# Kernel tuning notes

Measured on AMD Instinct MI355X. Metric: run time of the kernel, lower is better.

Reference implementation:

```python
import jax, jax.numpy as jnp
import numpy as np

EPS = 1e-8

def _conv(x, w, b=None):
    # NCHW conv, stride 1, SAME padding (k=3, pad=1)
    y = jax.lax.conv_general_dilated(x, w, (1, 1), 'SAME',
                                     dimension_numbers=('NCHW', 'OIHW', 'NCHW'))
    if b is not None:
        y = y + b[None, :, None, None]
    return y

def setup_inputs() -> dict:
    key = jax.random.key(0)
    ks = jax.random.split(key, 6)
    B, C, H, W = 512, 1024, 8, 8
    return {
        'x': jax.random.normal(ks[0], (B, C, H, W), jnp.float32),
        'w1_1': jax.random.normal(ks[1], (1, 1, 3, 3), jnp.float32) * 0.1,
        'w5': jax.random.normal(ks[2], (4, 2, 3, 3), jnp.float32) * 0.1,
        'b5': jax.random.normal(ks[3], (4,), jnp.float32) * 0.1,
        'w6': jax.random.normal(ks[4], (1, 4, 3, 3), jnp.float32) * 0.1,
        'b6': jax.random.normal(ks[5], (1,), jnp.float32) * 0.1,
    }

def reference(x, w1_1, w5, b5, w6, b6):
    B, C, H, W = x.shape  # H == W == 8 by module construction
    m = jnp.max(x, axis=1, keepdims=True)  # [B,1,H,W] channel max
    # 2x2 non-overlapping windows, torch unfold layout -> [B,1,(H/2)*(W/2),4]
    win = m.reshape(B, 1, H // 2, 2, W // 2, 2)
    win = win.transpose(0, 1, 2, 4, 3, 5).reshape(B, 1, (H // 2) * (W // 2), 4)
    # probabilistic pooling: clean inf/nan/negatives, sample per window
    winc = jnp.where(jnp.isinf(win) | jnp.isnan(win) | (win < 0), EPS, win)
    skey = jax.random.key(1)
    idx = jax.random.categorical(skey, winc, axis=-1)  # softmax(winc) multinomial
    mo2 = jnp.take_along_axis(winc, idx[..., None], axis=-1)[..., 0]
    mo2 = mo2.reshape(B, 1, H // 2, W // 2)
    # adaptive max/avg pool (4,4) on 8x8 == 2x2 pooling, reuse windows
    mo3 = win.max(axis=-1).reshape(B, 1, H // 2, W // 2)
    ao4 = win.mean(axis=-1).reshape(B, 1, H // 2, W // 2)
    out2 = 0.1 * mo2 + 0.6 * mo3 + 0.3 * ao4
    out2 = _conv(out2, w1_1)  # bias-free 1->1 conv
    out2 = jax.image.resize(out2, (B, 1, H, W), method='bilinear')  # align_corners=False
    out1 = jnp.concatenate([m, out2], axis=1)  # [B,2,H,W]
    gate = jax.nn.sigmoid(_conv(jax.nn.relu(_conv(out1, w5, b5)), w6, b6))  # [B,1,H,W]
    return jax.nn.relu(x * gate)
```

## Files before the change

kernel.cpp:

```cpp
#include <hip/hip_runtime.h>
#include <math.h>

#define C_DIM 1024
#define HW 64
#define NT_A 512
#define NT_B 256
#define F4_PER_BATCH 16384
#define EPSV 1e-8f
#define TINYF 1.17549435e-38f

__device__ __forceinline__ void threefry2x32_01(unsigned x0, unsigned x1,
                                                unsigned& o0, unsigned& o1) {
    const unsigned ks0 = 0u, ks1 = 1u, ks2 = 0x1BD11BDBu;
    x0 += ks0; x1 += ks1;
#define TF_R(r) { x0 += x1; x1 = (x1 << (r)) | (x1 >> (32 - (r))); x1 ^= x0; }
    TF_R(13) TF_R(15) TF_R(26) TF_R(6)
    x0 += ks1; x1 += ks2 + 1u;
    TF_R(17) TF_R(29) TF_R(16) TF_R(24)
    x0 += ks2; x1 += ks0 + 2u;
    TF_R(13) TF_R(15) TF_R(26) TF_R(6)
    x0 += ks0; x1 += ks1 + 3u;
    TF_R(17) TF_R(29) TF_R(16) TF_R(24)
    x0 += ks1; x1 += ks2 + 4u;
    TF_R(13) TF_R(15) TF_R(26) TF_R(6)
    x0 += ks2; x1 += ks0 + 5u;
#undef TF_R
    o0 = x0; o1 = x1;
}

__device__ __forceinline__ unsigned jax_random_bits(unsigned n) {
    unsigned o0, o1;
    threefry2x32_01(0u, n, o0, o1);
    return o0 ^ o1;
}

__device__ __forceinline__ bool bad_val(float v) {
    return ((__float_as_uint(v) & 0x7F800000u) == 0x7F800000u) || (v < 0.0f);
}

__global__ __launch_bounds__(NT_A) void sa_gate_kernel(
    const float* __restrict__ x,
    const float* __restrict__ w11,
    const float* __restrict__ w5,
    const float* __restrict__ b5,
    const float* __restrict__ w6,
    const float* __restrict__ b6,
    float* __restrict__ gate_out)
{
    const int b = blockIdx.x;
    const int t = threadIdx.x;

    const float4* __restrict__ xb = (const float4*)x + (size_t)b * F4_PER_BATCH;

    __shared__ float4 red[8 * 16];
    __shared__ float sm[64];
    __shared__ float sa16[16];
    __shared__ float sb16[16];
    __shared__ float so2[64];
    __shared__ float shid[4 * 64];

    float4 pm = make_float4(-INFINITY, -INFINITY, -INFINITY, -INFINITY);
#pragma unroll 16
    for (int i = 0; i < 32; ++i) {
        float4 v = xb[t + NT_A * i];
        pm.x = fmaxf(pm.x, v.x); pm.y = fmaxf(pm.y, v.y);
        pm.z = fmaxf(pm.z, v.z); pm.w = fmaxf(pm.w, v.w);
    }
#pragma unroll
    for (int off = 16; off <= 32; off <<= 1) {
        pm.x = fmaxf(pm.x, __shfl_xor(pm.x, off, 64));
        pm.y = fmaxf(pm.y, __shfl_xor(pm.y, off, 64));
        pm.z = fmaxf(pm.z, __shfl_xor(pm.z, off, 64));
        pm.w = fmaxf(pm.w, __shfl_xor(pm.w, off, 64));
    }
    const int wv = t >> 6, lane = t & 63;
    if (lane < 16) red[wv * 16 + lane] = pm;
    __syncthreads();
    if (t >= 64) return;

    if (t < 16) {
        float4 a = red[t];
#pragma unroll
        for (int w = 1; w < 8; ++w) {
            float4 o = red[w * 16 + t];
            a.x = fmaxf(a.x, o.x); a.y = fmaxf(a.y, o.y);
            a.z = fmaxf(a.z, o.z); a.w = fmaxf(a.w, o.w);
        }
        sm[t * 4 + 0] = a.x; sm[t * 4 + 1] = a.y;
        sm[t * 4 + 2] = a.z; sm[t * 4 + 3] = a.w;
    }
    __builtin_amdgcn_wave_barrier();

    if (t < 16) {
        int h2 = t >> 2, w2 = t & 3;
        float win[4], winc[4], sg[4];
#pragma unroll
        for (int j = 0; j < 4; ++j) {
            int hh = 2 * h2 + (j >> 1), ww = 2 * w2 + (j & 1);
            float v = sm[hh * 8 + ww];
            win[j] = v;
            winc[j] = bad_val(v) ? EPSV : v;
            unsigned n = (unsigned)(b * 64 + t * 4 + j);
            unsigned bits = jax_random_bits(n);
            float f = __uint_as_float(0x3F800000u | (bits >> 9)) - 1.0f;
            float u = fmaxf(TINYF, f + TINYF);
            sg[j] = -logf(-logf(u));
        }
        int idx = 0;
        float best = winc[0] + sg[0];
#pragma unroll
        for (int j = 1; j < 4; ++j) {
            float s = winc[j] + sg[j];
            if (s > best) { best = s; idx = j; }
        }
        float mo2 = winc[idx];
        float mo3 = fmaxf(fmaxf(win[0], win[1]), fmaxf(win[2], win[3]));
        float ssum = ((win[0] + win[1]) + win[2]) + win[3];
        float ao4 = ssum * 0.25f;
        sa16[t] = 0.1f * mo2 + 0.6f * mo3 + 0.3f * ao4;
    }
    __builtin_amdgcn_wave_barrier();

    if (t < 16) {
        int i = t >> 2, j = t & 3;
        float acc = 0.0f;
#pragma unroll
        for (int dy = -1; dy <= 1; ++dy) {
            int yy = i + dy;
            if (yy < 0 || yy > 3) continue;
#pragma unroll
            for (int dx = -1; dx <= 1; ++dx) {
                int xx = j + dx;
                if (xx < 0 || xx > 3) continue;
                acc += sa16[yy * 4 + xx] * w11[(dy + 1) * 3 + (dx + 1)];
            }
        }
        sb16[t] = acc;
    }
    __builtin_amdgcn_wave_barrier();

    {
        int y = t >> 3, xx2 = t & 7;
        float sy = (y + 0.5f) * 0.5f - 0.5f;
        float sx = (xx2 + 0.5f) * 0.5f - 0.5f;
        float fy = fminf(fmaxf(sy, 0.0f), 3.0f);
        float fx = fminf(fmaxf(sx, 0.0f), 3.0f);
        int iy0 = (int)floorf(fy); int iy1 = min(iy0 + 1, 3); float ry = fy - (float)iy0;
        int ix0 = (int)floorf(fx); int ix1 = min(ix0 + 1, 3); float rx = fx - (float)ix0;
        float v00 = sb16[iy0 * 4 + ix0], v01 = sb16[iy0 * 4 + ix1];
        float v10 = sb16[iy1 * 4 + ix0], v11 = sb16[iy1 * 4 + ix1];
        float top = v00 * (1.0f - rx) + v01 * rx;
        float bot = v10 * (1.0f - rx) + v11 * rx;
        so2[t] = top * (1.0f - ry) + bot * ry;
    }
    __builtin_amdgcn_wave_barrier();

    {
        int y = t >> 3, x2 = t & 7;
        float a0 = b5[0], a1 = b5[1], a2 = b5[2], a3 = b5[3];
#pragma unroll
        for (int dy = -1; dy <= 1; ++dy) {
            int yy = y + dy;
            if (yy < 0 || yy > 7) continue;
#pragma unroll
            for (int dx = -1; dx <= 1; ++dx) {
                int xx = x2 + dx;
                if (xx < 0 || xx > 7) continue;
                float i0 = sm[yy * 8 + xx];
                float i1 = so2[yy * 8 + xx];
                int kk = (dy + 1) * 3 + (dx + 1);
                a0 += i0 * w5[0 * 18 + kk] + i1 * w5[0 * 18 + 9 + kk];
                a1 += i0 * w5[1 * 18 + kk] + i1 * w5[1 * 18 + 9 + kk];
                a2 += i0 * w5[2 * 18 + kk] + i1 * w5[2 * 18 + 9 + kk];
                a3 += i0 * w5[3 * 18 + kk] + i1 * w5[3 * 18 + 9 + kk];
            }
        }
        shid[0 * 64 + t] = fmaxf(a0, 0.0f);
        shid[1 * 64 + t] = fmaxf(a1, 0.0f);
        shid[2 * 64 + t] = fmaxf(a2, 0.0f);
        shid[3 * 64 + t] = fmaxf(a3, 0.0f);
    }
    __builtin_amdgcn_wave_barrier();

    {
        int y = t >> 3, x2 = t & 7;
        float acc = b6[0];
#pragma unroll
        for (int dy = -1; dy <= 1; ++dy) {
            int yy = y + dy;
            if (yy < 0 || yy > 7) continue;
#pragma unroll
            for (int dx = -1; dx <= 1; ++dx) {
                int xx = x2 + dx;
                if (xx < 0 || xx > 7) continue;
                int kk = (dy + 1) * 3 + (dx + 1);
                int p = yy * 8 + xx;
                acc += shid[0 * 64 + p] * w6[0 + kk]
                     + shid[1 * 64 + p] * w6[9 + kk]
                     + shid[2 * 64 + p] * w6[18 + kk]
                     + shid[3 * 64 + p] * w6[27 + kk];
            }
        }
        gate_out[b * 64 + t] = 1.0f / (1.0f + expf(-acc));
    }
}

__global__ __launch_bounds__(NT_B) void sa_apply_kernel(
    const float* __restrict__ x,
    const float* __restrict__ gate,
    float* __restrict__ out)
{
    const int bid = blockIdx.x;
    const int t = threadIdx.x;
    const int b = bid >> 2;
    const size_t base = (size_t)bid * 4096;

    const float4* __restrict__ x4 = (const float4*)x;
    float4* __restrict__ o4 = (float4*)out;

    const float4 gv = ((const float4*)(gate + b * 64))[t & 15];

#pragma unroll 8
    for (int i = 0; i < 16; ++i) {
        size_t idx = base + t + NT_B * i;
        float4 v = x4[idx];
        float4 o;
        o.x = fmaxf(v.x * gv.x, 0.0f);
        o.y = fmaxf(v.y * gv.y, 0.0f);
        o.z = fmaxf(v.z * gv.z, 0.0f);
        o.w = fmaxf(v.w * gv.w, 0.0f);
        o4[idx] = o;
    }
}

extern "C" void kernel_launch(void* const* d_in, const int* in_sizes, int n_in,
                              void* d_out, int out_size, void* d_ws, size_t ws_size,
                              hipStream_t stream) {
    const float* x   = (const float*)d_in[0];
    const float* w11 = (const float*)d_in[1];
    const float* w5  = (const float*)d_in[2];
    const float* b5  = (const float*)d_in[3];
    const float* w6  = (const float*)d_in[4];
    const float* b6  = (const float*)d_in[5];
    float* out  = (float*)d_out;
    float* gate = (float*)d_ws;

    int B = in_sizes[0] / (C_DIM * HW);
    sa_gate_kernel<<<dim3(B), dim3(NT_A), 0, stream>>>(x, w11, w5, b5, w6, b6, gate);
    sa_apply_kernel<<<dim3(B * 4), dim3(NT_B), 0, stream>>>(x, gate, out);
}
```

Measured before the change: 259.6 us.

## Fuse gate computation and apply into one kernel holding x in registers

```diff
diff --git a/kernel.cpp b/kernel.cpp
--- a/kernel.cpp
+++ b/kernel.cpp
@@ -3,9 +3,9 @@
 
 #define C_DIM 1024
 #define HW 64
-#define NT_A 512
-#define NT_B 256
+#define NT 1024
 #define F4_PER_BATCH 16384
+#define PER_T 16
 #define EPSV 1e-8f
 #define TINYF 1.17549435e-38f
 
@@ -38,33 +38,36 @@
     return ((__float_as_uint(v) & 0x7F800000u) == 0x7F800000u) || (v < 0.0f);
 }
 
-__global__ __launch_bounds__(NT_A) void sa_gate_kernel(
+__global__ __launch_bounds__(NT) void sa_fused_kernel(
     const float* __restrict__ x,
     const float* __restrict__ w11,
     const float* __restrict__ w5,
     const float* __restrict__ b5,
     const float* __restrict__ w6,
     const float* __restrict__ b6,
-    float* __restrict__ gate_out)
+    float* __restrict__ out)
 {
     const int b = blockIdx.x;
     const int t = threadIdx.x;
 
     const float4* __restrict__ xb = (const float4*)x + (size_t)b * F4_PER_BATCH;
-
-    __shared__ float4 red[8 * 16];
+    float4* __restrict__ ob = (float4*)out + (size_t)b * F4_PER_BATCH;
+
+    __shared__ float4 red[16 * 16];
     __shared__ float sm[64];
     __shared__ float sa16[16];
     __shared__ float sb16[16];
     __shared__ float so2[64];
     __shared__ float shid[4 * 64];
-
+    __shared__ __align__(16) float sgate[64];
+
+    float4 xv[PER_T];
     float4 pm = make_float4(-INFINITY, -INFINITY, -INFINITY, -INFINITY);
-#pragma unroll 16
-    for (int i = 0; i < 32; ++i) {
-        float4 v = xb[t + NT_A * i];
-        pm.x = fmaxf(pm.x, v.x); pm.y = fmaxf(pm.y, v.y);
-        pm.z = fmaxf(pm.z, v.z); pm.w = fmaxf(pm.w, v.w);
+#pragma unroll
+    for (int i = 0; i < PER_T; ++i) {
+        xv[i] = xb[t + NT * i];
+        pm.x = fmaxf(pm.x, xv[i].x); pm.y = fmaxf(pm.y, xv[i].y);
+        pm.z = fmaxf(pm.z, xv[i].z); pm.w = fmaxf(pm.w, xv[i].w);
     }
 #pragma unroll
     for (int off = 16; off <= 32; off <<= 1) {
@@ -76,160 +79,146 @@
     const int wv = t >> 6, lane = t & 63;
     if (lane < 16) red[wv * 16 + lane] = pm;
     __syncthreads();
-    if (t >= 64) return;
-
-    if (t < 16) {
-        float4 a = red[t];
-#pragma unroll
-        for (int w = 1; w < 8; ++w) {
-            float4 o = red[w * 16 + t];
-            a.x = fmaxf(a.x, o.x); a.y = fmaxf(a.y, o.y);
-            a.z = fmaxf(a.z, o.z); a.w = fmaxf(a.w, o.w);
-        }
-        sm[t * 4 + 0] = a.x; sm[t * 4 + 1] = a.y;
-        sm[t * 4 + 2] = a.z; sm[t * 4 + 3] = a.w;
-    }
-    __builtin_amdgcn_wave_barrier();
-
-    if (t < 16) {
-        int h2 = t >> 2, w2 = t & 3;
-        float win[4], winc[4], sg[4];
-#pragma unroll
-        for (int j = 0; j < 4; ++j) {
-            int hh = 2 * h2 + (j >> 1), ww = 2 * w2 + (j & 1);
-            float v = sm[hh * 8 + ww];
-            win[j] = v;
-            winc[j] = bad_val(v) ? EPSV : v;
-            unsigned n = (unsigned)(b * 64 + t * 4 + j);
-            unsigned bits = jax_random_bits(n);
-            float f = __uint_as_float(0x3F800000u | (bits >> 9)) - 1.0f;
-            float u = fmaxf(TINYF, f + TINYF);
-            sg[j] = -logf(-logf(u));
-        }
-        int idx = 0;
-        float best = winc[0] + sg[0];
-#pragma unroll
-        for (int j = 1; j < 4; ++j) {
-            float s = winc[j] + sg[j];
-            if (s > best) { best = s; idx = j; }
-        }
-        float mo2 = winc[idx];
-        float mo3 = fmaxf(fmaxf(win[0], win[1]), fmaxf(win[2], win[3]));
-        float ssum = ((win[0] + win[1]) + win[2]) + win[3];
-        float ao4 = ssum * 0.25f;
-        sa16[t] = 0.1f * mo2 + 0.6f * mo3 + 0.3f * ao4;
-    }
-    __builtin_amdgcn_wave_barrier();
-
-    if (t < 16) {
-        int i = t >> 2, j = t & 3;
-        float acc = 0.0f;
-#pragma unroll
-        for (int dy = -1; dy <= 1; ++dy) {
-            int yy = i + dy;
-            if (yy < 0 || yy > 3) continue;
-#pragma unroll
-            for (int dx = -1; dx <= 1; ++dx) {
-                int xx = j + dx;
-                if (xx < 0 || xx > 3) continue;
-                acc += sa16[yy * 4 + xx] * w11[(dy + 1) * 3 + (dx + 1)];
-            }
-        }
-        sb16[t] = acc;
-    }
-    __builtin_amdgcn_wave_barrier();
-
-    {
-        int y = t >> 3, xx2 = t & 7;
-        float sy = (y + 0.5f) * 0.5f - 0.5f;
-        float sx = (xx2 + 0.5f) * 0.5f - 0.5f;
-        float fy = fminf(fmaxf(sy, 0.0f), 3.0f);
-        float fx = fminf(fmaxf(sx, 0.0f), 3.0f);
-        int iy0 = (int)floorf(fy); int iy1 = min(iy0 + 1, 3); float ry = fy - (float)iy0;
-        int ix0 = (int)floorf(fx); int ix1 = min(ix0 + 1, 3); float rx = fx - (float)ix0;
-        float v00 = sb16[iy0 * 4 + ix0], v01 = sb16[iy0 * 4 + ix1];
-        float v10 = sb16[iy1 * 4 + ix0], v11 = sb16[iy1 * 4 + ix1];
-        float top = v00 * (1.0f - rx) + v01 * rx;
-        float bot = v10 * (1.0f - rx) + v11 * rx;
-        so2[t] = top * (1.0f - ry) + bot * ry;
-    }
-    __builtin_amdgcn_wave_barrier();
-
-    {
-        int y = t >> 3, x2 = t & 7;
-        float a0 = b5[0], a1 = b5[1], a2 = b5[2], a3 = b5[3];
-#pragma unroll
-        for (int dy = -1; dy <= 1; ++dy) {
-            int yy = y + dy;
-            if (yy < 0 || yy > 7) continue;
-#pragma unroll
-            for (int dx = -1; dx <= 1; ++dx) {
-                int xx = x2 + dx;
-                if (xx < 0 || xx > 7) continue;
-                float i0 = sm[yy * 8 + xx];
-                float i1 = so2[yy * 8 + xx];
-                int kk = (dy + 1) * 3 + (dx + 1);
-                a0 += i0 * w5[0 * 18 + kk] + i1 * w5[0 * 18 + 9 + kk];
-                a1 += i0 * w5[1 * 18 + kk] + i1 * w5[1 * 18 + 9 + kk];
-                a2 += i0 * w5[2 * 18 + kk] + i1 * w5[2 * 18 + 9 + kk];
-                a3 += i0 * w5[3 * 18 + kk] + i1 * w5[3 * 18 + 9 + kk];
-            }
-        }
-        shid[0 * 64 + t] = fmaxf(a0, 0.0f);
-        shid[1 * 64 + t] = fmaxf(a1, 0.0f);
-        shid[2 * 64 + t] = fmaxf(a2, 0.0f);
-        shid[3 * 64 + t] = fmaxf(a3, 0.0f);
-    }
-    __builtin_amdgcn_wave_barrier();
-
-    {
-        int y = t >> 3, x2 = t & 7;
-        float acc = b6[0];
-#pragma unroll
-        for (int dy = -1; dy <= 1; ++dy) {
-            int yy = y + dy;
-            if (yy < 0 || yy > 7) continue;
-#pragma unroll
-            for (int dx = -1; dx <= 1; ++dx) {
-                int xx = x2 + dx;
-                if (xx < 0 || xx > 7) continue;
-                int kk = (dy + 1) * 3 + (dx + 1);
-                int p = yy * 8 + xx;
-                acc += shid[0 * 64 + p] * w6[0 + kk]
-                     + shid[1 * 64 + p] * w6[9 + kk]
-                     + shid[2 * 64 + p] * w6[18 + kk]
-                     + shid[3 * 64 + p] * w6[27 + kk];
-            }
-        }
-        gate_out[b * 64 + t] = 1.0f / (1.0f + expf(-acc));
-    }
-}
-
-__global__ __launch_bounds__(NT_B) void sa_apply_kernel(
-    const float* __restrict__ x,
-    const float* __restrict__ gate,
-    float* __restrict__ out)
-{
-    const int bid = blockIdx.x;
-    const int t = threadIdx.x;
-    const int b = bid >> 2;
-    const size_t base = (size_t)bid * 4096;
-
-    const float4* __restrict__ x4 = (const float4*)x;
-    float4* __restrict__ o4 = (float4*)out;
-
-    const float4 gv = ((const float4*)(gate + b * 64))[t & 15];
-
-#pragma unroll 8
-    for (int i = 0; i < 16; ++i) {
-        size_t idx = base + t + NT_B * i;
-        float4 v = x4[idx];
+
+    if (t < 64) {
+        if (t < 16) {
+            float4 a = red[t];
+#pragma unroll
+            for (int w = 1; w < 16; ++w) {
+                float4 o = red[w * 16 + t];
+                a.x = fmaxf(a.x, o.x); a.y = fmaxf(a.y, o.y);
+                a.z = fmaxf(a.z, o.z); a.w = fmaxf(a.w, o.w);
+            }
+            sm[t * 4 + 0] = a.x; sm[t * 4 + 1] = a.y;
+            sm[t * 4 + 2] = a.z; sm[t * 4 + 3] = a.w;
+        }
+        __builtin_amdgcn_wave_barrier();
+
+        if (t < 16) {
+            int h2 = t >> 2, w2 = t & 3;
+            float win[4], winc[4], sg[4];
+#pragma unroll
+            for (int j = 0; j < 4; ++j) {
+                int hh = 2 * h2 + (j >> 1), ww = 2 * w2 + (j & 1);
+                float v = sm[hh * 8 + ww];
+                win[j] = v;
+                winc[j] = bad_val(v) ? EPSV : v;
+                unsigned n = (unsigned)(b * 64 + t * 4 + j);
+                unsigned bits = jax_random_bits(n);
+                float f = __uint_as_float(0x3F800000u | (bits >> 9)) - 1.0f;
+                float u = fmaxf(TINYF, f + TINYF);
+                sg[j] = -logf(-logf(u));
+            }
+            int idx = 0;
+            float best = winc[0] + sg[0];
+#pragma unroll
+            for (int j = 1; j < 4; ++j) {
+                float s = winc[j] + sg[j];
+                if (s > best) { best = s; idx = j; }
+            }
+            float mo2 = winc[idx];
+            float mo3 = fmaxf(fmaxf(win[0], win[1]), fmaxf(win[2], win[3]));
+            float ssum = ((win[0] + win[1]) + win[2]) + win[3];
+            float ao4 = ssum * 0.25f;
+            sa16[t] = 0.1f * mo2 + 0.6f * mo3 + 0.3f * ao4;
+        }
+        __builtin_amdgcn_wave_barrier();
+
+        if (t < 16) {
+            int i = t >> 2, j = t & 3;
+            float acc = 0.0f;
+#pragma unroll
+            for (int dy = -1; dy <= 1; ++dy) {
+                int yy = i + dy;
+                if (yy < 0 || yy > 3) continue;
+#pragma unroll
+                for (int dx = -1; dx <= 1; ++dx) {
+                    int xx = j + dx;
+                    if (xx < 0 || xx > 3) continue;
+                    acc += sa16[yy * 4 + xx] * w11[(dy + 1) * 3 + (dx + 1)];
+                }
+            }
+            sb16[t] = acc;
+        }
+        __builtin_amdgcn_wave_barrier();
+
+        {
+            int y = t >> 3, xx2 = t & 7;
+            float sy = (y + 0.5f) * 0.5f - 0.5f;
+            float sx = (xx2 + 0.5f) * 0.5f - 0.5f;
+            float fy = fminf(fmaxf(sy, 0.0f), 3.0f);
+            float fx = fminf(fmaxf(sx, 0.0f), 3.0f);
+            int iy0 = (int)floorf(fy); int iy1 = min(iy0 + 1, 3); float ry = fy - (float)iy0;
+            int ix0 = (int)floorf(fx); int ix1 = min(ix0 + 1, 3); float rx = fx - (float)ix0;
+            float v00 = sb16[iy0 * 4 + ix0], v01 = sb16[iy0 * 4 + ix1];
+            float v10 = sb16[iy1 * 4 + ix0], v11 = sb16[iy1 * 4 + ix1];
+            float top = v00 * (1.0f - rx) + v01 * rx;
+            float bot = v10 * (1.0f - rx) + v11 * rx;
+            so2[t] = top * (1.0f - ry) + bot * ry;
+        }
+        __builtin_amdgcn_wave_barrier();
+
+        {
+            int y = t >> 3, x2 = t & 7;
+            float a0 = b5[0], a1 = b5[1], a2 = b5[2], a3 = b5[3];
+#pragma unroll
+            for (int dy = -1; dy <= 1; ++dy) {
+                int yy = y + dy;
+                if (yy < 0 || yy > 7) continue;
+#pragma unroll
+                for (int dx = -1; dx <= 1; ++dx) {
+                    int xx = x2 + dx;
+                    if (xx < 0 || xx > 7) continue;
+                    float i0 = sm[yy * 8 + xx];
+                    float i1 = so2[yy * 8 + xx];
+                    int kk = (dy + 1) * 3 + (dx + 1);
+                    a0 += i0 * w5[0 * 18 + kk] + i1 * w5[0 * 18 + 9 + kk];
+                    a1 += i0 * w5[1 * 18 + kk] + i1 * w5[1 * 18 + 9 + kk];
+                    a2 += i0 * w5[2 * 18 + kk] + i1 * w5[2 * 18 + 9 + kk];
+                    a3 += i0 * w5[3 * 18 + kk] + i1 * w5[3 * 18 + 9 + kk];
+                }
+            }
+            shid[0 * 64 + t] = fmaxf(a0, 0.0f);
+            shid[1 * 64 + t] = fmaxf(a1, 0.0f);
+            shid[2 * 64 + t] = fmaxf(a2, 0.0f);
+            shid[3 * 64 + t] = fmaxf(a3, 0.0f);
+        }
+        __builtin_amdgcn_wave_barrier();
+
+        {
+            int y = t >> 3, x2 = t & 7;
+            float acc = b6[0];
+#pragma unroll
+            for (int dy = -1; dy <= 1; ++dy) {
+                int yy = y + dy;
+                if (yy < 0 || yy > 7) continue;
+#pragma unroll
+                for (int dx = -1; dx <= 1; ++dx) {
+                    int xx = x2 + dx;
+                    if (xx < 0 || xx > 7) continue;
+                    int kk = (dy + 1) * 3 + (dx + 1);
+                    int p = yy * 8 + xx;
+                    acc += shid[0 * 64 + p] * w6[0 + kk]
+                         + shid[1 * 64 + p] * w6[9 + kk]
+                         + shid[2 * 64 + p] * w6[18 + kk]
+                         + shid[3 * 64 + p] * w6[27 + kk];
+                }
+            }
+            sgate[t] = 1.0f / (1.0f + expf(-acc));
+        }
+    }
+    __syncthreads();
+
+    const float4 gv = ((const float4*)sgate)[t & 15];
+#pragma unroll
+    for (int i = 0; i < PER_T; ++i) {
+        float4 v = xv[i];
         float4 o;
         o.x = fmaxf(v.x * gv.x, 0.0f);
         o.y = fmaxf(v.y * gv.y, 0.0f);
         o.z = fmaxf(v.z * gv.z, 0.0f);
         o.w = fmaxf(v.w * gv.w, 0.0f);
-        o4[idx] = o;
+        ob[t + NT * i] = o;
     }
 }
 
@@ -243,9 +232,7 @@
     const float* w6  = (const float*)d_in[4];
     const float* b6  = (const float*)d_in[5];
     float* out  = (float*)d_out;
-    float* gate = (float*)d_ws;
 
     int B = in_sizes[0] / (C_DIM * HW);
-    sa_gate_kernel<<<dim3(B), dim3(NT_A), 0, stream>>>(x, w11, w5, b5, w6, b6, gate);
-    sa_apply_kernel<<<dim3(B * 4), dim3(NT_B), 0, stream>>>(x, gate, out);
-}
+    sa_fused_kernel<<<dim3(B), dim3(NT), 0, stream>>>(x, w11, w5, b5, w6, b6, out);
+}
```

Result: faster. 247.7 us (-4.6%).

## Split channel-max into partial-reduction kernel and separate gate computation kernel

Applied to the files above, without the earlier changes.

```diff
diff --git a/kernel.cpp b/kernel.cpp
--- a/kernel.cpp
+++ b/kernel.cpp
@@ -3,11 +3,11 @@
 
 #define C_DIM 1024
 #define HW 64
-#define NT_A 512
-#define NT_B 256
-#define F4_PER_BATCH 16384
+#define F4B 16384
 #define EPSV 1e-8f
 #define TINYF 1.17549435e-38f
+
+typedef float f32x4_t __attribute__((ext_vector_type(4)));
 
 __device__ __forceinline__ void threefry2x32_01(unsigned x0, unsigned x1,
                                                 unsigned& o0, unsigned& o1) {
@@ -34,90 +34,102 @@
     return o0 ^ o1;
 }
 
+__device__ __forceinline__ float gumbel01(unsigned n) {
+    unsigned bits = jax_random_bits(n);
+    float f = __uint_as_float(0x3F800000u | (bits >> 9)) - 1.0f;
+    float u = fmaxf(TINYF, f + TINYF);
+    return -logf(-logf(u));
+}
+
 __device__ __forceinline__ bool bad_val(float v) {
     return ((__float_as_uint(v) & 0x7F800000u) == 0x7F800000u) || (v < 0.0f);
 }
 
-__global__ __launch_bounds__(NT_A) void sa_gate_kernel(
+__global__ __launch_bounds__(256) void sa_maxpart_kernel(
     const float* __restrict__ x,
+    float* __restrict__ part)
+{
+    const int bid = blockIdx.x;
+    const int t = threadIdx.x;
+    const int b = bid >> 2, q = bid & 3;
+
+    const float4* __restrict__ xq =
+        (const float4*)x + (size_t)b * F4B + (size_t)q * 4096;
+
+    float4 pm = make_float4(-INFINITY, -INFINITY, -INFINITY, -INFINITY);
+#pragma unroll
+    for (int i = 0; i < 16; ++i) {
+        float4 v = xq[t + 256 * i];
+        pm.x = fmaxf(pm.x, v.x); pm.y = fmaxf(pm.y, v.y);
+        pm.z = fmaxf(pm.z, v.z); pm.w = fmaxf(pm.w, v.w);
+    }
+#pragma unroll
+    for (int off = 16; off <= 32; off <<= 1) {
+        pm.x = fmaxf(pm.x, __shfl_xor(pm.x, off, 64));
+        pm.y = fmaxf(pm.y, __shfl_xor(pm.y, off, 64));
+        pm.z = fmaxf(pm.z, __shfl_xor(pm.z, off, 64));
+        pm.w = fmaxf(pm.w, __shfl_xor(pm.w, off, 64));
+    }
+    __shared__ float4 red[4 * 16];
+    const int wv = t >> 6, lane = t & 63;
+    if (lane < 16) red[wv * 16 + lane] = pm;
+    __syncthreads();
+    if (t < 16) {
+        float4 a = red[t];
+#pragma unroll
+        for (int w = 1; w < 4; ++w) {
+            float4 o = red[w * 16 + t];
+            a.x = fmaxf(a.x, o.x); a.y = fmaxf(a.y, o.y);
+            a.z = fmaxf(a.z, o.z); a.w = fmaxf(a.w, o.w);
+        }
+        float* dst = part + ((size_t)b * 4 + q) * 64 + t * 4;
+        dst[0] = a.x; dst[1] = a.y; dst[2] = a.z; dst[3] = a.w;
+    }
+}
+
+__global__ __launch_bounds__(64) void sa_middle_kernel(
+    const float* __restrict__ part,
     const float* __restrict__ w11,
     const float* __restrict__ w5,
     const float* __restrict__ b5,
     const float* __restrict__ w6,
     const float* __restrict__ b6,
-    float* __restrict__ gate_out)
+    float* __restrict__ gate)
 {
     const int b = blockIdx.x;
     const int t = threadIdx.x;
 
-    const float4* __restrict__ xb = (const float4*)x + (size_t)b * F4_PER_BATCH;
-
-    __shared__ float4 red[8 * 16];
-    __shared__ float sm[64];
-    __shared__ float sa16[16];
-    __shared__ float sb16[16];
-    __shared__ float so2[64];
-    __shared__ float shid[4 * 64];
-
-    float4 pm = make_float4(-INFINITY, -INFINITY, -INFINITY, -INFINITY);
-#pragma unroll 16
-    for (int i = 0; i < 32; ++i) {
-        float4 v = xb[t + NT_A * i];
-        pm.x = fmaxf(pm.x, v.x); pm.y = fmaxf(pm.y, v.y);
-        pm.z = fmaxf(pm.z, v.z); pm.w = fmaxf(pm.w, v.w);
-    }
-#pragma unroll
-    for (int off = 16; off <= 32; off <<= 1) {
-        pm.x = fmaxf(pm.x, __shfl_xor(pm.x, off, 64));
-        pm.y = fmaxf(pm.y, __shfl_xor(pm.y, off, 64));
-        pm.z = fmaxf(pm.z, __shfl_xor(pm.z, off, 64));
-        pm.w = fmaxf(pm.w, __shfl_xor(pm.w, off, 64));
-    }
-    const int wv = t >> 6, lane = t & 63;
-    if (lane < 16) red[wv * 16 + lane] = pm;
-    __syncthreads();
-    if (t >= 64) return;
-
-    if (t < 16) {
-        float4 a = red[t];
-#pragma unroll
-        for (int w = 1; w < 8; ++w) {
-            float4 o = red[w * 16 + t];
-            a.x = fmaxf(a.x, o.x); a.y = fmaxf(a.y, o.y);
-            a.z = fmaxf(a.z, o.z); a.w = fmaxf(a.w, o.w);
-        }
-        sm[t * 4 + 0] = a.x; sm[t * 4 + 1] = a.y;
-        sm[t * 4 + 2] = a.z; sm[t * 4 + 3] = a.w;
-    }
-    __builtin_amdgcn_wave_barrier();
-
-    if (t < 16) {
-        int h2 = t >> 2, w2 = t & 3;
-        float win[4], winc[4], sg[4];
-#pragma unroll
-        for (int j = 0; j < 4; ++j) {
-            int hh = 2 * h2 + (j >> 1), ww = 2 * w2 + (j & 1);
-            float v = sm[hh * 8 + ww];
-            win[j] = v;
-            winc[j] = bad_val(v) ? EPSV : v;
-            unsigned n = (unsigned)(b * 64 + t * 4 + j);
-            unsigned bits = jax_random_bits(n);
-            float f = __uint_as_float(0x3F800000u | (bits >> 9)) - 1.0f;
-            float u = fmaxf(TINYF, f + TINYF);
-            sg[j] = -logf(-logf(u));
-        }
-        int idx = 0;
-        float best = winc[0] + sg[0];
-#pragma unroll
-        for (int j = 1; j < 4; ++j) {
-            float s = winc[j] + sg[j];
-            if (s > best) { best = s; idx = j; }
-        }
-        float mo2 = winc[idx];
-        float mo3 = fmaxf(fmaxf(win[0], win[1]), fmaxf(win[2], win[3]));
-        float ssum = ((win[0] + win[1]) + win[2]) + win[3];
-        float ao4 = ssum * 0.25f;
-        sa16[t] = 0.1f * mo2 + 0.6f * mo3 + 0.3f * ao4;
+    __shared__ float sm[64], sa16[16], sb16[16], so2[64], shid[4 * 64];
+
+    const float* pb = part + (size_t)b * 256;
+    float m = fmaxf(fmaxf(pb[t], pb[64 + t]), fmaxf(pb[128 + t], pb[192 + t]));
+    sm[t] = m;
+    const float sgum = gumbel01((unsigned)(b * 64 + t));
+    __builtin_amdgcn_wave_barrier();
+
+    {
+        int w = t >> 2, j = t & 3;
+        int hh = 2 * (w >> 2) + (j >> 1), ww = 2 * (w & 3) + (j & 1);
+        float v = sm[hh * 8 + ww];
+        float wc = bad_val(v) ? EPSV : v;
+        float s = wc + sgum;
+        int bi = j;
+        float bwc = wc;
+        float mx = v;
+        float ssum = v;
+#pragma unroll
+        for (int mk = 1; mk <= 2; mk <<= 1) {
+            float s2   = __shfl_xor(s, mk, 64);
+            int   bi2  = __shfl_xor(bi, mk, 64);
+            float bwc2 = __shfl_xor(bwc, mk, 64);
+            float mx2  = __shfl_xor(mx, mk, 64);
+            float ss2  = __shfl_xor(ssum, mk, 64);
+            bool take = (s2 > s) || (s2 == s && bi2 < bi);
+            if (take) { s = s2; bi = bi2; bwc = bwc2; }
+            mx = fmaxf(mx, mx2);
+            ssum += ss2;
+        }
+        if (j == 0) sa16[w] = 0.1f * bwc + 0.6f * mx + 0.3f * (ssum * 0.25f);
     }
     __builtin_amdgcn_wave_barrier();
 
@@ -201,11 +213,11 @@
                      + shid[3 * 64 + p] * w6[27 + kk];
             }
         }
-        gate_out[b * 64 + t] = 1.0f / (1.0f + expf(-acc));
-    }
-}
-
-__global__ __launch_bounds__(NT_B) void sa_apply_kernel(
+        gate[(size_t)b * 64 + t] = 1.0f / (1.0f + expf(-acc));
+    }
+}
+
+__global__ __launch_bounds__(256) void sa_apply_kernel(
     const float* __restrict__ x,
     const float* __restrict__ gate,
     float* __restrict__ out)
@@ -218,18 +230,18 @@
     const float4* __restrict__ x4 = (const float4*)x;
     float4* __restrict__ o4 = (float4*)out;
 
-    const float4 gv = ((const float4*)(gate + b * 64))[t & 15];
-
-#pragma unroll 8
+    const float4 gv = ((const float4*)(gate + (size_t)b * 64))[t & 15];
+
+#pragma unroll
     for (int i = 0; i < 16; ++i) {
-        size_t idx = base + t + NT_B * i;
+        size_t idx = base + t + 256 * i;
         float4 v = x4[idx];
-        float4 o;
+        f32x4_t o;
         o.x = fmaxf(v.x * gv.x, 0.0f);
         o.y = fmaxf(v.y * gv.y, 0.0f);
         o.z = fmaxf(v.z * gv.z, 0.0f);
         o.w = fmaxf(v.w * gv.w, 0.0f);
-        o4[idx] = o;
+        __builtin_nontemporal_store(o, (f32x4_t*)&o4[idx]);
     }
 }
 
@@ -243,9 +255,12 @@
     const float* w6  = (const float*)d_in[4];
     const float* b6  = (const float*)d_in[5];
     float* out  = (float*)d_out;
+
+    int B = in_sizes[0] / (C_DIM * HW);
     float* gate = (float*)d_ws;
-
-    int B = in_sizes[0] / (C_DIM * HW);
-    sa_gate_kernel<<<dim3(B), dim3(NT_A), 0, stream>>>(x, w11, w5, b5, w6, b6, gate);
-    sa_apply_kernel<<<dim3(B * 4), dim3(NT_B), 0, stream>>>(x, gate, out);
-}
+    float* part = (float*)d_ws + (size_t)B * 64;
+
+    sa_maxpart_kernel<<<dim3(B * 4), dim3(256), 0, stream>>>(x, part);
+    sa_middle_kernel<<<dim3(B), dim3(64), 0, stream>>>(part, w11, w5, b5, w6, b6, gate);
+    sa_apply_kernel<<<dim3(B * 4), dim3(256), 0, stream>>>(x, gate, out);
+}
```

Result: no change. 262.4 us (+1.1%).
